# Performance work log

Hardware: AMD Instinct MI355X
Metric: run time of the kernel (lower is better)

## Reference

```python
import jax, jax.numpy as jnp
import numpy as np

B, S, D = 2, 2048, 1024
H, HD = 16, 64


def setup_inputs() -> dict:
    key = jax.random.key(0)
    ks = jax.random.split(key, 6)
    hidden_states = jax.random.normal(ks[0], (B, S, D), dtype=jnp.float32)
    c_attn_w = jax.random.normal(ks[1], (D, 3 * D), dtype=jnp.float32) * 0.02
    c_attn_b = jnp.zeros((3 * D,), dtype=jnp.float32)
    c_proj_w = jax.random.normal(ks[2], (D, D), dtype=jnp.float32) * 0.02
    c_proj_b = jnp.zeros((D,), dtype=jnp.float32)
    basis = jax.random.normal(ks[3], (H, HD, HD), dtype=jnp.float32) * 0.1
    projectors = jnp.einsum('hdr,her->hde', basis, basis)  # basis @ basis.T per head
    return {
        'hidden_states': hidden_states,
        'c_attn_w': c_attn_w,
        'c_attn_b': c_attn_b,
        'c_proj_w': c_proj_w,
        'c_proj_b': c_proj_b,
        'projectors': projectors,
    }


def reference(hidden_states, c_attn_w, c_attn_b, c_proj_w, c_proj_b, projectors):
    # GPT2 Conv1D: out = x @ W + b
    qkv = hidden_states @ c_attn_w + c_attn_b  # [B,S,3D]
    q, k, v = jnp.split(qkv, 3, axis=-1)
    # split heads -> [B,H,S,HD]
    def split_heads(t):
        return t.reshape(B, S, H, HD).transpose(0, 2, 1, 3)
    q, k, v = split_heads(q), split_heads(k), split_heads(v)
    scores = jnp.einsum('bhqd,bhkd->bhqk', q, k) / jnp.sqrt(jnp.float32(HD))
    causal = jnp.tril(jnp.ones((S, S), dtype=bool))
    scores = jnp.where(causal, scores, jnp.finfo(scores.dtype).min)
    probs = jax.nn.softmax(scores, axis=-1)
    attn = jnp.einsum('bhqk,bhkd->bhqd', probs, v)  # [B,H,S,HD]
    # per-head basis projector applied to attention output
    attn = jnp.einsum('bhsd,hde->bhse', attn, projectors)
    # merge heads -> [B,S,D]
    attn = attn.transpose(0, 2, 1, 3).reshape(B, S, D)
    out = attn @ c_proj_w + c_proj_b
    return out
```

## Files before the change

kernel.cpp:

```cpp
#include <hip/hip_runtime.h>

typedef __attribute__((ext_vector_type(8))) short bhalf8;
typedef __attribute__((ext_vector_type(4))) float f32x4;
typedef __attribute__((ext_vector_type(8))) unsigned short u16x8;
typedef __attribute__((ext_vector_type(4))) unsigned short u16x4;

#define BDIM 2
#define SDIM 2048
#define DDIM 1024
#define HDIM 16
#define HDHD 64

__device__ __forceinline__ unsigned short f2bf(float f) {
  unsigned u = __builtin_bit_cast(unsigned, f);
  u += 0x7fffu + ((u >> 16) & 1u);
  return (unsigned short)(u >> 16);
}
__device__ __forceinline__ float bf2f(unsigned short u) {
  return __builtin_bit_cast(float, (unsigned)u << 16);
}

__global__ __launch_bounds__(256) void cvt_hidden(const float* __restrict__ x,
                                                  unsigned short* __restrict__ y) {
  size_t i = ((size_t)blockIdx.x * 256 + threadIdx.x) * 4;
  f32x4 v = *(const f32x4*)(x + i);
  u16x4 o;
  o[0] = f2bf(v[0]); o[1] = f2bf(v[1]); o[2] = f2bf(v[2]); o[3] = f2bf(v[3]);
  *(u16x4*)(y + i) = o;
}

__global__ __launch_bounds__(256) void transpose_cvt(const float* __restrict__ W,
                                                     unsigned short* __restrict__ Wt,
                                                     int R, int C) {
  __shared__ float tl[32][33];
  int rt = blockIdx.x * 32, ct = blockIdx.y * 32;
  int r8 = threadIdx.x >> 5, c = threadIdx.x & 31;
#pragma unroll
  for (int i = 0; i < 4; i++)
    tl[r8 + i * 8][c] = W[(size_t)(rt + r8 + i * 8) * C + ct + c];
  __syncthreads();
#pragma unroll
  for (int i = 0; i < 4; i++)
    Wt[(size_t)(ct + r8 + i * 8) * R + rt + c] = f2bf(tl[c][r8 + i * 8]);
}

__global__ __launch_bounds__(256) void make_wproj(const float* __restrict__ proj,
                                                  const float* __restrict__ wproj,
                                                  unsigned short* __restrict__ WT) {
  int h = blockIdx.x, ot = blockIdx.y * 64;
  __shared__ float Pl[64][65];
  __shared__ float Wl[64][65];
  int t = threadIdx.x;
#pragma unroll
  for (int i = 0; i < 16; i++) {
    int idx = t + 256 * i;
    int a = idx >> 6, bc = idx & 63;
    Pl[a][bc] = proj[(size_t)h * 4096 + idx];
    Wl[a][bc] = wproj[(size_t)(h * 64 + a) * 1024 + ot + bc];
  }
  __syncthreads();
  int d = t & 63, ob = t >> 6;
#pragma unroll
  for (int i = 0; i < 16; i++) {
    int o = ob + i * 4;
    float acc = 0.f;
#pragma unroll
    for (int e = 0; e < 64; e++) acc += Pl[d][e] * Wl[e][o];
    WT[(size_t)(ot + o) * 1024 + h * 64 + d] = f2bf(acc);
  }
}

template <int EPI>
__global__ __launch_bounds__(256) void gemm_bt(
    const unsigned short* __restrict__ A, const unsigned short* __restrict__ Bt,
    const float* __restrict__ bias, float* __restrict__ Cf,
    unsigned short* __restrict__ q, unsigned short* __restrict__ k,
    unsigned short* __restrict__ v, int M, int N, int K) {
  __shared__ unsigned short As[128][72];
  __shared__ unsigned short Bs[128][72];
  const int tid = threadIdx.x;
  const int m0 = blockIdx.y * 128, n0 = blockIdx.x * 128;
  f32x4 acc[4][4];
#pragma unroll
  for (int m = 0; m < 4; m++)
#pragma unroll
    for (int n = 0; n < 4; n++) acc[m][n] = f32x4{0.f, 0.f, 0.f, 0.f};
  const int w = tid >> 6, lane = tid & 63;
  const int wr = (w >> 1) * 64, wc = (w & 1) * 64;
  const int lrow = lane & 15, lk = (lane >> 4) * 8;

  for (int kt = 0; kt < K; kt += 64) {
    __syncthreads();
#pragma unroll
    for (int i = 0; i < 4; i++) {
      int cch = tid + 256 * i;
      int r = cch >> 3, c8 = cch & 7;
      *(u16x8*)(&As[r][c8 * 8]) = *(const u16x8*)(A + (size_t)(m0 + r) * K + kt + c8 * 8);
      *(u16x8*)(&Bs[r][c8 * 8]) = *(const u16x8*)(Bt + (size_t)(n0 + r) * K + kt + c8 * 8);
    }
    __syncthreads();
#pragma unroll
    for (int kk = 0; kk < 2; kk++) {
      bhalf8 af[4], bfr[4];
#pragma unroll
      for (int m = 0; m < 4; m++) af[m] = *(const bhalf8*)(&As[wr + m * 16 + lrow][kk * 32 + lk]);
#pragma unroll
      for (int n = 0; n < 4; n++) bfr[n] = *(const bhalf8*)(&Bs[wc + n * 16 + lrow][kk * 32 + lk]);
#pragma unroll
      for (int m = 0; m < 4; m++)
#pragma unroll
        for (int n = 0; n < 4; n++)
          acc[m][n] = __builtin_amdgcn_mfma_f32_16x16x32_bf16(af[m], bfr[n], acc[m][n], 0, 0, 0);
    }
  }
  const int g = lane >> 4, il = lane & 15;
#pragma unroll
  for (int m = 0; m < 4; m++) {
    int rowb = wr + m * 16 + 4 * g;
#pragma unroll
    for (int n = 0; n < 4; n++) {
      int col = n0 + wc + n * 16 + il;
      float bs = bias[col];
#pragma unroll
      for (int r = 0; r < 4; r++) {
        int row = m0 + rowb + r;
        float val = acc[m][n][r] + bs;
        if (EPI == 0) {
          int which = col >> 10, hh = (col >> 6) & 15, hd = col & 63;
          int b = row >> 11, s = row & 2047;
          size_t idx = ((size_t)(b * 16 + hh) * SDIM + s) * HDHD + hd;
          unsigned short bv = f2bf(which == 0 ? val * 0.1803368801f : val);
          if (which == 0) q[idx] = bv;
          else if (which == 1) k[idx] = bv;
          else v[idx] = bv;
        } else {
          Cf[(size_t)row * N + col] = val;
        }
      }
    }
  }
}

__global__ __launch_bounds__(128, 3) void attn_partial(const unsigned short* __restrict__ Q,
                                                       const unsigned short* __restrict__ Kb,
                                                       const unsigned short* __restrict__ Vb,
                                                       unsigned short* __restrict__ PO,
                                                       float2* __restrict__ ML) {
  __shared__ unsigned short Ks[64][72];
  __shared__ unsigned short Vt[64][72];
  __shared__ unsigned short Ps[2][32][72];
  const int bh = blockIdx.x;
  const int qt = 31 - blockIdx.y;
  const int seg = blockIdx.z;
  const int a = qt >> 3, bq = qt & 7;
  const int nseg = a + 1;
  if (seg >= nseg) return;
  const int k0 = seg * 8;
  const int k1 = min(k0 + 8, qt + 1);

  const int tid = threadIdx.x;
  const int w = tid >> 6, lane = tid & 63;
  const int g = lane >> 4, il = lane & 15;
  const int qbase = qt * 64 + w * 32;
  const size_t bhS = (size_t)bh * SDIM;

  bhalf8 qf[2][2];
#pragma unroll
  for (int f = 0; f < 2; f++) {
    const unsigned short* qp = Q + (bhS + qbase + f * 16 + il) * HDHD + g * 8;
    qf[f][0] = *(const bhalf8*)(qp);
    qf[f][1] = *(const bhalf8*)(qp + 32);
  }
  f32x4 oacc[2][4];
#pragma unroll
  for (int f = 0; f < 2; f++)
#pragma unroll
    for (int i = 0; i < 4; i++) oacc[f][i] = f32x4{0.f, 0.f, 0.f, 0.f};
  float mrun[2] = {-1e30f, -1e30f}, lrun[2] = {0.f, 0.f};

  const int krow = tid >> 1;
  const int kchk = (tid & 1) * 32;
  const int vd0 = (tid & 31) * 2;
  const int vkg = (tid >> 5) * 16;

  u16x8 kr[4];
  unsigned vr[16];
  {
    const size_t kb0 = (bhS + (size_t)k0 * 64) * HDHD;
    const unsigned short* ksrc = Kb + kb0 + krow * HDHD + kchk;
#pragma unroll
    for (int i = 0; i < 4; i++) kr[i] = *(const u16x8*)(ksrc + i * 8);
    const unsigned short* vsrc = Vb + kb0 + (size_t)vkg * HDHD + vd0;
#pragma unroll
    for (int i = 0; i < 16; i++) vr[i] = *(const unsigned*)(vsrc + i * HDHD);
  }

  for (int kt = k0; kt < k1; kt++) {
    __syncthreads();
#pragma unroll
    for (int i = 0; i < 4; i++) *(u16x8*)(&Ks[krow][kchk + i * 8]) = kr[i];
    {
      u16x8 lo0, lo1, hi0, hi1;
#pragma unroll
      for (int i = 0; i < 8; i++) {
        lo0[i] = (unsigned short)(vr[i] & 0xffffu); hi0[i] = (unsigned short)(vr[i] >> 16);
      }
#pragma unroll
      for (int i = 0; i < 8; i++) {
        lo1[i] = (unsigned short)(vr[8 + i] & 0xffffu); hi1[i] = (unsigned short)(vr[8 + i] >> 16);
      }
      *(u16x8*)(&Vt[vd0][vkg]) = lo0;     *(u16x8*)(&Vt[vd0][vkg + 8]) = lo1;
      *(u16x8*)(&Vt[vd0 + 1][vkg]) = hi0; *(u16x8*)(&Vt[vd0 + 1][vkg + 8]) = hi1;
    }
    if (kt + 1 < k1) {
      const size_t kbn = (bhS + (size_t)(kt + 1) * 64) * HDHD;
      const unsigned short* ksrc = Kb + kbn + krow * HDHD + kchk;
#pragma unroll
      for (int i = 0; i < 4; i++) kr[i] = *(const u16x8*)(ksrc + i * 8);
      const unsigned short* vsrc = Vb + kbn + (size_t)vkg * HDHD + vd0;
#pragma unroll
      for (int i = 0; i < 16; i++) vr[i] = *(const unsigned*)(vsrc + i * HDHD);
    }
    __syncthreads();
    f32x4 s[2][4];
#pragma unroll
    for (int f = 0; f < 2; f++)
#pragma unroll
      for (int c = 0; c < 4; c++) s[f][c] = f32x4{0.f, 0.f, 0.f, 0.f};
#pragma unroll
    for (int c = 0; c < 4; c++) {
      bhalf8 kf0 = *(const bhalf8*)(&Ks[c * 16 + il][g * 8]);
      bhalf8 kf1 = *(const bhalf8*)(&Ks[c * 16 + il][32 + g * 8]);
#pragma unroll
      for (int f = 0; f < 2; f++) {
        s[f][c] = __builtin_amdgcn_mfma_f32_16x16x32_bf16(kf0, qf[f][0], s[f][c], 0, 0, 0);
        s[f][c] = __builtin_amdgcn_mfma_f32_16x16x32_bf16(kf1, qf[f][1], s[f][c], 0, 0, 0);
      }
    }
    const bool diag = (kt == qt);
    float lmax[2];
#pragma unroll
    for (int f = 0; f < 2; f++) {
      const int thr = w * 32 + f * 16 + il;
      float lm = -1e30f;
#pragma unroll
      for (int c = 0; c < 4; c++)
#pragma unroll
        for (int r = 0; r < 4; r++) {
          float v = s[f][c][r];
          if (diag && (c * 16 + 4 * g + r > thr)) v = -1e30f;
          s[f][c][r] = v;
          lm = fmaxf(lm, v);
        }
      lm = fmaxf(lm, __shfl_xor(lm, 16));
      lm = fmaxf(lm, __shfl_xor(lm, 32));
      lmax[f] = lm;
    }
    if (!__all((lmax[0] <= mrun[0] + 7.f) && (lmax[1] <= mrun[1] + 7.f))) {
#pragma unroll
      for (int f = 0; f < 2; f++) {
        float mn = fmaxf(mrun[f], lmax[f]);
        float sc = exp2f(mrun[f] - mn);
        mrun[f] = mn;
        lrun[f] *= sc;
#pragma unroll
        for (int df = 0; df < 4; df++)
#pragma unroll
          for (int r = 0; r < 4; r++) oacc[f][df][r] *= sc;
      }
    }
#pragma unroll
    for (int f = 0; f < 2; f++) {
      float rs = 0.f;
#pragma unroll
      for (int c = 0; c < 4; c++) {
        u16x4 pk;
#pragma unroll
        for (int r = 0; r < 4; r++) {
          float pv = exp2f(s[f][c][r] - mrun[f]);
          rs += pv;
          pk[r] = f2bf(pv);
        }
        *(u16x4*)(&Ps[w][f * 16 + il][c * 16 + 4 * g]) = pk;
      }
      rs += __shfl_xor(rs, 16);
      rs += __shfl_xor(rs, 32);
      lrun[f] += rs;
    }
#pragma unroll
    for (int kk = 0; kk < 2; kk++) {
      bhalf8 pf0 = *(const bhalf8*)(&Ps[w][il][kk * 32 + g * 8]);
      bhalf8 pf1 = *(const bhalf8*)(&Ps[w][16 + il][kk * 32 + g * 8]);
#pragma unroll
      for (int df = 0; df < 4; df++) {
        bhalf8 vf = *(const bhalf8*)(&Vt[df * 16 + il][kk * 32 + g * 8]);
        oacc[0][df] = __builtin_amdgcn_mfma_f32_16x16x32_bf16(vf, pf0, oacc[0][df], 0, 0, 0);
        oacc[1][df] = __builtin_amdgcn_mfma_f32_16x16x32_bf16(vf, pf1, oacc[1][df], 0, 0, 0);
      }
    }
  }
  const int pidx = bh * 80 + 4 * a * (a + 1) + bq * (a + 1) + seg;
  __syncthreads();
#pragma unroll
  for (int f = 0; f < 2; f++) {
    float inv = 1.f / lrun[f];
#pragma unroll
    for (int df = 0; df < 4; df++) {
      u16x4 o;
#pragma unroll
      for (int r = 0; r < 4; r++) o[r] = f2bf(oacc[f][df][r] * inv);
      *(u16x4*)(&Ks[w * 32 + f * 16 + il][df * 16 + 4 * g]) = o;
    }
  }
  if (g == 0) {
#pragma unroll
    for (int f = 0; f < 2; f++)
      ML[(size_t)pidx * 64 + w * 32 + f * 16 + il] = make_float2(mrun[f], lrun[f]);
  }
  __syncthreads();
  {
    const int row = tid >> 1, half = (tid & 1) * 32;
    unsigned short* dst = PO + (size_t)pidx * 4096 + (size_t)row * 64 + half;
#pragma unroll
    for (int c8 = 0; c8 < 4; c8++)
      *(u16x8*)(dst + c8 * 8) = *(const u16x8*)(&Ks[row][half + c8 * 8]);
  }
}

__global__ __launch_bounds__(256) void attn_reduce(const unsigned short* __restrict__ PO,
                                                   const float2* __restrict__ ML,
                                                   unsigned short* __restrict__ Om) {
  const int bh = blockIdx.x, qt = blockIdx.y;
  const int a = qt >> 3, bq = qt & 7;
  const int nseg = a + 1;
  const int base = bh * 80 + 4 * a * (a + 1) + bq * (a + 1);
  const int t = threadIdx.x;
  const int r = t >> 2, dc = (t & 3) * 16;
  float2 mls[4];
  float M = -1e30f;
#pragma unroll
  for (int s = 0; s < 4; s++) {
    if (s < nseg) { mls[s] = ML[(size_t)(base + s) * 64 + r]; M = fmaxf(M, mls[s].x); }
  }
  float L = 0.f;
  float O[16];
#pragma unroll
  for (int j = 0; j < 16; j++) O[j] = 0.f;
#pragma unroll
  for (int s = 0; s < 4; s++) {
    if (s < nseg) {
      float wgt = mls[s].y * exp2f(mls[s].x - M);
      L += wgt;
      const unsigned short* p = PO + (size_t)(base + s) * 4096 + r * 64 + dc;
      u16x8 p0 = *(const u16x8*)p, p1 = *(const u16x8*)(p + 8);
#pragma unroll
      for (int j = 0; j < 8; j++) O[j] += wgt * bf2f(p0[j]);
#pragma unroll
      for (int j = 0; j < 8; j++) O[8 + j] += wgt * bf2f(p1[j]);
    }
  }
  float inv = 1.f / L;
  const int b = bh >> 4, h = bh & 15;
  size_t orow = ((size_t)b * SDIM + qt * 64 + r) * DDIM + h * HDHD + dc;
  u16x8 o0, o1;
#pragma unroll
  for (int j = 0; j < 8; j++) o0[j] = f2bf(O[j] * inv);
#pragma unroll
  for (int j = 0; j < 8; j++) o1[j] = f2bf(O[8 + j] * inv);
  *(u16x8*)(Om + orow) = o0;
  *(u16x8*)(Om + orow + 8) = o1;
}

__global__ __launch_bounds__(128, 2) void attn_direct(const unsigned short* __restrict__ Q,
                                                      const unsigned short* __restrict__ Kb,
                                                      const unsigned short* __restrict__ Vb,
                                                      unsigned short* __restrict__ Om) {
  __shared__ unsigned short Ks[64][72];
  __shared__ unsigned short Vt[64][72];
  __shared__ unsigned short Ps[2][32][72];
  const int bh = blockIdx.x;
  const int qt = 31 - blockIdx.y;
  const int tid = threadIdx.x;
  const int w = tid >> 6, lane = tid & 63;
  const int g = lane >> 4, il = lane & 15;
  const int qbase = qt * 64 + w * 32;
  const size_t bhS = (size_t)bh * SDIM;
  bhalf8 qf[2][2];
#pragma unroll
  for (int f = 0; f < 2; f++) {
    const unsigned short* qp = Q + (bhS + qbase + f * 16 + il) * HDHD + g * 8;
    qf[f][0] = *(const bhalf8*)(qp);
    qf[f][1] = *(const bhalf8*)(qp + 32);
  }
  f32x4 oacc[2][4];
#pragma unroll
  for (int f = 0; f < 2; f++)
#pragma unroll
    for (int i = 0; i < 4; i++) oacc[f][i] = f32x4{0.f, 0.f, 0.f, 0.f};
  float mrun[2] = {-1e30f, -1e30f}, lrun[2] = {0.f, 0.f};
  const int krow = tid >> 1, kchk = (tid & 1) * 32;
  const int vd0 = (tid & 31) * 2, vkg = (tid >> 5) * 16;
  const int nt = qt + 1;
  for (int kt = 0; kt < nt; kt++) {
    const size_t kbase = (bhS + (size_t)kt * 64) * HDHD;
    __syncthreads();
    {
      const unsigned short* src = Kb + kbase + krow * HDHD + kchk;
#pragma unroll
      for (int i = 0; i < 4; i++) *(u16x8*)(&Ks[krow][kchk + i * 8]) = *(const u16x8*)(src + i * 8);
    }
    {
      const unsigned short* vsrc = Vb + kbase + (size_t)vkg * HDHD + vd0;
      u16x8 lo0, lo1, hi0, hi1;
#pragma unroll
      for (int i = 0; i < 8; i++) {
        unsigned vv = *(const unsigned*)(vsrc + i * HDHD);
        lo0[i] = (unsigned short)(vv & 0xffffu); hi0[i] = (unsigned short)(vv >> 16);
      }
#pragma unroll
      for (int i = 0; i < 8; i++) {
        unsigned vv = *(const unsigned*)(vsrc + (8 + i) * HDHD);
        lo1[i] = (unsigned short)(vv & 0xffffu); hi1[i] = (unsigned short)(vv >> 16);
      }
      *(u16x8*)(&Vt[vd0][vkg]) = lo0;     *(u16x8*)(&Vt[vd0][vkg + 8]) = lo1;
      *(u16x8*)(&Vt[vd0 + 1][vkg]) = hi0; *(u16x8*)(&Vt[vd0 + 1][vkg + 8]) = hi1;
    }
    __syncthreads();
    f32x4 s[2][4];
#pragma unroll
    for (int f = 0; f < 2; f++)
#pragma unroll
      for (int c = 0; c < 4; c++) s[f][c] = f32x4{0.f, 0.f, 0.f, 0.f};
#pragma unroll
    for (int c = 0; c < 4; c++) {
      bhalf8 kf0 = *(const bhalf8*)(&Ks[c * 16 + il][g * 8]);
      bhalf8 kf1 = *(const bhalf8*)(&Ks[c * 16 + il][32 + g * 8]);
#pragma unroll
      for (int f = 0; f < 2; f++) {
        s[f][c] = __builtin_amdgcn_mfma_f32_16x16x32_bf16(kf0, qf[f][0], s[f][c], 0, 0, 0);
        s[f][c] = __builtin_amdgcn_mfma_f32_16x16x32_bf16(kf1, qf[f][1], s[f][c], 0, 0, 0);
      }
    }
    const bool diag = (kt == qt);
#pragma unroll
    for (int f = 0; f < 2; f++) {
      const int thr = w * 32 + f * 16 + il;
      float p[4][4];
      float lmax = -1e30f;
#pragma unroll
      for (int c = 0; c < 4; c++)
#pragma unroll
        for (int r = 0; r < 4; r++) {
          float v = s[f][c][r];
          if (diag && (c * 16 + 4 * g + r > thr)) v = -1e30f;
          p[c][r] = v;
          lmax = fmaxf(lmax, v);
        }
      lmax = fmaxf(lmax, __shfl_xor(lmax, 16));
      lmax = fmaxf(lmax, __shfl_xor(lmax, 32));
      float mn = fmaxf(mrun[f], lmax);
      float sc = exp2f(mrun[f] - mn);
      mrun[f] = mn;
      float rs = 0.f;
#pragma unroll
      for (int c = 0; c < 4; c++)
#pragma unroll
        for (int r = 0; r < 4; r++) { p[c][r] = exp2f(p[c][r] - mn); rs += p[c][r]; }
      rs += __shfl_xor(rs, 16);
      rs += __shfl_xor(rs, 32);
      lrun[f] = lrun[f] * sc + rs;
#pragma unroll
      for (int df = 0; df < 4; df++)
#pragma unroll
        for (int r = 0; r < 4; r++) oacc[f][df][r] *= sc;
#pragma unroll
      for (int c = 0; c < 4; c++) {
        u16x4 pk;
#pragma unroll
        for (int r = 0; r < 4; r++) pk[r] = f2bf(p[c][r]);
        *(u16x4*)(&Ps[w][f * 16 + il][c * 16 + 4 * g]) = pk;
      }
    }
#pragma unroll
    for (int kk = 0; kk < 2; kk++) {
      bhalf8 pf0 = *(const bhalf8*)(&Ps[w][il][kk * 32 + g * 8]);
      bhalf8 pf1 = *(const bhalf8*)(&Ps[w][16 + il][kk * 32 + g * 8]);
#pragma unroll
      for (int df = 0; df < 4; df++) {
        bhalf8 vf = *(const bhalf8*)(&Vt[df * 16 + il][kk * 32 + g * 8]);
        oacc[0][df] = __builtin_amdgcn_mfma_f32_16x16x32_bf16(vf, pf0, oacc[0][df], 0, 0, 0);
        oacc[1][df] = __builtin_amdgcn_mfma_f32_16x16x32_bf16(vf, pf1, oacc[1][df], 0, 0, 0);
      }
    }
  }
  __syncthreads();
#pragma unroll
  for (int f = 0; f < 2; f++) {
    float inv = 1.f / lrun[f];
#pragma unroll
    for (int df = 0; df < 4; df++) {
      u16x4 o;
#pragma unroll
      for (int r = 0; r < 4; r++) o[r] = f2bf(oacc[f][df][r] * inv);
      *(u16x4*)(&Ks[w * 32 + f * 16 + il][df * 16 + 4 * g]) = o;
    }
  }
  __syncthreads();
  {
    const int row = tid >> 1, half = (tid & 1) * 32;
    const int b = bh >> 4, h = bh & 15;
    size_t obase = ((size_t)b * SDIM + qt * 64 + row) * DDIM + h * HDHD + half;
#pragma unroll
    for (int c8 = 0; c8 < 4; c8++)
      *(u16x8*)(Om + obase + c8 * 8) = *(const u16x8*)(&Ks[row][half + c8 * 8]);
  }
}

extern "C" void kernel_launch(void* const* d_in, const int* in_sizes, int n_in,
                              void* d_out, int out_size, void* d_ws, size_t ws_size,
                              hipStream_t stream) {
  const float* hidden = (const float*)d_in[0];
  const float* attn_w = (const float*)d_in[1];
  const float* attn_b = (const float*)d_in[2];
  const float* proj_w = (const float*)d_in[3];
  const float* proj_b = (const float*)d_in[4];
  const float* projectors = (const float*)d_in[5];
  float* out = (float*)d_out;
  char* ws = (char*)d_ws;
  (void)in_sizes; (void)n_in; (void)out_size;

  unsigned short* hseq   = (unsigned short*)(ws);
  unsigned short* wqkvT  = (unsigned short*)(ws + 8388608);
  unsigned short* qb     = (unsigned short*)(ws + 14680064);
  unsigned short* kb     = (unsigned short*)(ws + 23068672);
  unsigned short* vb     = (unsigned short*)(ws + 31457280);
  unsigned short* attnM  = (unsigned short*)(ws + 39845888);
  unsigned short* wprojT = (unsigned short*)(ws + 48234496);
  unsigned short* PO     = (unsigned short*)(ws + 50331648);
  float2*         ML2    = (float2*)(ws + 71303168);
  const size_t ws_needed = 71303168 + 1310720;

  cvt_hidden<<<dim3(4096), dim3(256), 0, stream>>>(hidden, hseq);
  transpose_cvt<<<dim3(32, 96), dim3(256), 0, stream>>>(attn_w, wqkvT, 1024, 3072);
  make_wproj<<<dim3(16, 16), dim3(256), 0, stream>>>(projectors, proj_w, wprojT);
  gemm_bt<0><<<dim3(24, 32), dim3(256), 0, stream>>>(hseq, wqkvT, attn_b, nullptr,
                                                     qb, kb, vb, 4096, 3072, 1024);
  if (ws_size >= ws_needed) {
    attn_partial<<<dim3(32, 32, 4), dim3(128), 0, stream>>>(qb, kb, vb, PO, ML2);
    attn_reduce<<<dim3(32, 32), dim3(256), 0, stream>>>(PO, ML2, attnM);
  } else {
    attn_direct<<<dim3(32, 32), dim3(128), 0, stream>>>(qb, kb, vb, attnM);
  }
  gemm_bt<1><<<dim3(8, 32), dim3(256), 0, stream>>>(attnM, wprojT, proj_b, out,
                                                    nullptr, nullptr, nullptr, 4096, 1024, 1024);
}
```

Measured before the change: 171.7 us.

## Double-buffer GEMM tiles via direct global-to-LDS loads and attention K/V LDS

The bf16 GEMM now stages A and B tiles straight from global memory into LDS with global_load_lds into two ping-pong buffers. The next k-tile is issued before the MFMA work on the current one, leaving one barrier per iteration instead of two. The attention partial kernel double-buffers its K and V^T LDS tiles, which removes one barrier per key tile and lets the next tile's global loads overlap the current tile's compute. The GEMM's LDS rows lose their padding (64 instead of 72 elements), so fragment reads may hit bank conflicts.

```diff
diff --git a/kernel.cpp b/kernel.cpp
--- a/kernel.cpp
+++ b/kernel.cpp
@@ -10,6 +10,11 @@
 #define DDIM 1024
 #define HDIM 16
 #define HDHD 64
+
+#define GLD16(gaddr, laddr)                                                          \
+  __builtin_amdgcn_global_load_lds(                                                  \
+      (const __attribute__((address_space(1))) unsigned int*)(gaddr),                \
+      (__attribute__((address_space(3))) unsigned int*)(laddr), 16, 0, 0)
 
 __device__ __forceinline__ unsigned short f2bf(float f) {
   unsigned u = __builtin_bit_cast(unsigned, f);
@@ -76,8 +81,8 @@
     const float* __restrict__ bias, float* __restrict__ Cf,
     unsigned short* __restrict__ q, unsigned short* __restrict__ k,
     unsigned short* __restrict__ v, int M, int N, int K) {
-  __shared__ unsigned short As[128][72];
-  __shared__ unsigned short Bs[128][72];
+  __shared__ unsigned short As[2][128 * 64];
+  __shared__ unsigned short Bs[2][128 * 64];
   const int tid = threadIdx.x;
   const int m0 = blockIdx.y * 128, n0 = blockIdx.x * 128;
   f32x4 acc[4][4];
@@ -88,30 +93,40 @@
   const int w = tid >> 6, lane = tid & 63;
   const int wr = (w >> 1) * 64, wc = (w & 1) * 64;
   const int lrow = lane & 15, lk = (lane >> 4) * 8;
-
+  const int srow = tid >> 3, sc8 = (tid & 7) * 8;
+
+  auto STAGE = [&](int bi, int kt) {
+#pragma unroll
+    for (int i = 0; i < 4; i++) {
+      int c = tid + 256 * i;
+      int r = srow + i * 32;
+      GLD16(A + (size_t)(m0 + r) * K + kt + sc8, &As[bi][c * 8]);
+      GLD16(Bt + (size_t)(n0 + r) * K + kt + sc8, &Bs[bi][c * 8]);
+    }
+  };
+
+  STAGE(0, 0);
+  __syncthreads();
+  int cur = 0;
   for (int kt = 0; kt < K; kt += 64) {
-    __syncthreads();
-#pragma unroll
-    for (int i = 0; i < 4; i++) {
-      int cch = tid + 256 * i;
-      int r = cch >> 3, c8 = cch & 7;
-      *(u16x8*)(&As[r][c8 * 8]) = *(const u16x8*)(A + (size_t)(m0 + r) * K + kt + c8 * 8);
-      *(u16x8*)(&Bs[r][c8 * 8]) = *(const u16x8*)(Bt + (size_t)(n0 + r) * K + kt + c8 * 8);
-    }
-    __syncthreads();
+    if (kt + 64 < K) STAGE(cur ^ 1, kt + 64);
 #pragma unroll
     for (int kk = 0; kk < 2; kk++) {
       bhalf8 af[4], bfr[4];
 #pragma unroll
-      for (int m = 0; m < 4; m++) af[m] = *(const bhalf8*)(&As[wr + m * 16 + lrow][kk * 32 + lk]);
-#pragma unroll
-      for (int n = 0; n < 4; n++) bfr[n] = *(const bhalf8*)(&Bs[wc + n * 16 + lrow][kk * 32 + lk]);
+      for (int m = 0; m < 4; m++)
+        af[m] = *(const bhalf8*)(&As[cur][(wr + m * 16 + lrow) * 64 + kk * 32 + lk]);
+#pragma unroll
+      for (int n = 0; n < 4; n++)
+        bfr[n] = *(const bhalf8*)(&Bs[cur][(wc + n * 16 + lrow) * 64 + kk * 32 + lk]);
 #pragma unroll
       for (int m = 0; m < 4; m++)
 #pragma unroll
         for (int n = 0; n < 4; n++)
           acc[m][n] = __builtin_amdgcn_mfma_f32_16x16x32_bf16(af[m], bfr[n], acc[m][n], 0, 0, 0);
     }
+    __syncthreads();
+    cur ^= 1;
   }
   const int g = lane >> 4, il = lane & 15;
 #pragma unroll
@@ -146,8 +161,8 @@
                                                        const unsigned short* __restrict__ Vb,
                                                        unsigned short* __restrict__ PO,
                                                        float2* __restrict__ ML) {
-  __shared__ unsigned short Ks[64][72];
-  __shared__ unsigned short Vt[64][72];
+  __shared__ unsigned short Ks[2][64][72];
+  __shared__ unsigned short Vt[2][64][72];
   __shared__ unsigned short Ps[2][32][72];
   const int bh = blockIdx.x;
   const int qt = 31 - blockIdx.y;
@@ -185,20 +200,22 @@
 
   u16x8 kr[4];
   unsigned vr[16];
-  {
-    const size_t kb0 = (bhS + (size_t)k0 * 64) * HDHD;
-    const unsigned short* ksrc = Kb + kb0 + krow * HDHD + kchk;
+  auto LOADT = [&](int kt) {
+    const size_t kb = (bhS + (size_t)kt * 64) * HDHD;
+    const unsigned short* ksrc = Kb + kb + krow * HDHD + kchk;
 #pragma unroll
     for (int i = 0; i < 4; i++) kr[i] = *(const u16x8*)(ksrc + i * 8);
-    const unsigned short* vsrc = Vb + kb0 + (size_t)vkg * HDHD + vd0;
+    const unsigned short* vsrc = Vb + kb + (size_t)vkg * HDHD + vd0;
 #pragma unroll
     for (int i = 0; i < 16; i++) vr[i] = *(const unsigned*)(vsrc + i * HDHD);
-  }
+  };
+
+  LOADT(k0);
 
   for (int kt = k0; kt < k1; kt++) {
-    __syncthreads();
-#pragma unroll
-    for (int i = 0; i < 4; i++) *(u16x8*)(&Ks[krow][kchk + i * 8]) = kr[i];
+    const int bi = kt & 1;
+#pragma unroll
+    for (int i = 0; i < 4; i++) *(u16x8*)(&Ks[bi][krow][kchk + i * 8]) = kr[i];
     {
       u16x8 lo0, lo1, hi0, hi1;
 #pragma unroll
@@ -209,19 +226,11 @@
       for (int i = 0; i < 8; i++) {
         lo1[i] = (unsigned short)(vr[8 + i] & 0xffffu); hi1[i] = (unsigned short)(vr[8 + i] >> 16);
       }
-      *(u16x8*)(&Vt[vd0][vkg]) = lo0;     *(u16x8*)(&Vt[vd0][vkg + 8]) = lo1;
-      *(u16x8*)(&Vt[vd0 + 1][vkg]) = hi0; *(u16x8*)(&Vt[vd0 + 1][vkg + 8]) = hi1;
-    }
-    if (kt + 1 < k1) {
-      const size_t kbn = (bhS + (size_t)(kt + 1) * 64) * HDHD;
-      const unsigned short* ksrc = Kb + kbn + krow * HDHD + kchk;
-#pragma unroll
-      for (int i = 0; i < 4; i++) kr[i] = *(const u16x8*)(ksrc + i * 8);
-      const unsigned short* vsrc = Vb + kbn + (size_t)vkg * HDHD + vd0;
-#pragma unroll
-      for (int i = 0; i < 16; i++) vr[i] = *(const unsigned*)(vsrc + i * HDHD);
+      *(u16x8*)(&Vt[bi][vd0][vkg]) = lo0;     *(u16x8*)(&Vt[bi][vd0][vkg + 8]) = lo1;
+      *(u16x8*)(&Vt[bi][vd0 + 1][vkg]) = hi0; *(u16x8*)(&Vt[bi][vd0 + 1][vkg + 8]) = hi1;
     }
     __syncthreads();
+    if (kt + 1 < k1) LOADT(kt + 1);
     f32x4 s[2][4];
 #pragma unroll
     for (int f = 0; f < 2; f++)
@@ -229,8 +238,8 @@
       for (int c = 0; c < 4; c++) s[f][c] = f32x4{0.f, 0.f, 0.f, 0.f};
 #pragma unroll
     for (int c = 0; c < 4; c++) {
-      bhalf8 kf0 = *(const bhalf8*)(&Ks[c * 16 + il][g * 8]);
-      bhalf8 kf1 = *(const bhalf8*)(&Ks[c * 16 + il][32 + g * 8]);
+      bhalf8 kf0 = *(const bhalf8*)(&Ks[bi][c * 16 + il][g * 8]);
+      bhalf8 kf1 = *(const bhalf8*)(&Ks[bi][c * 16 + il][32 + g * 8]);
 #pragma unroll
       for (int f = 0; f < 2; f++) {
         s[f][c] = __builtin_amdgcn_mfma_f32_16x16x32_bf16(kf0, qf[f][0], s[f][c], 0, 0, 0);
@@ -293,7 +302,7 @@
       bhalf8 pf1 = *(const bhalf8*)(&Ps[w][16 + il][kk * 32 + g * 8]);
 #pragma unroll
       for (int df = 0; df < 4; df++) {
-        bhalf8 vf = *(const bhalf8*)(&Vt[df * 16 + il][kk * 32 + g * 8]);
+        bhalf8 vf = *(const bhalf8*)(&Vt[bi][df * 16 + il][kk * 32 + g * 8]);
         oacc[0][df] = __builtin_amdgcn_mfma_f32_16x16x32_bf16(vf, pf0, oacc[0][df], 0, 0, 0);
         oacc[1][df] = __builtin_amdgcn_mfma_f32_16x16x32_bf16(vf, pf1, oacc[1][df], 0, 0, 0);
       }
@@ -309,7 +318,7 @@
       u16x4 o;
 #pragma unroll
       for (int r = 0; r < 4; r++) o[r] = f2bf(oacc[f][df][r] * inv);
-      *(u16x4*)(&Ks[w * 32 + f * 16 + il][df * 16 + 4 * g]) = o;
+      *(u16x4*)(&Ks[0][w * 32 + f * 16 + il][df * 16 + 4 * g]) = o;
     }
   }
   if (g == 0) {
@@ -323,7 +332,7 @@
     unsigned short* dst = PO + (size_t)pidx * 4096 + (size_t)row * 64 + half;
 #pragma unroll
     for (int c8 = 0; c8 < 4; c8++)
-      *(u16x8*)(dst + c8 * 8) = *(const u16x8*)(&Ks[row][half + c8 * 8]);
+      *(u16x8*)(dst + c8 * 8) = *(const u16x8*)(&Ks[0][row][half + c8 * 8]);
   }
 }
 
```

Result: slower. 191.9 us (+11.7%).
